# Kernel tuning notes

Hardware: AMD Instinct MI355X
Metric: run time of the kernel (lower is better)

The kernel has to match this reference:

```python
import jax, jax.numpy as jnp
import numpy as np

N = 200000      # nodes
E = 1600000     # edges
B = 1000        # graphs
SD = 64         # state_dim
AD = 32         # action_dim
H = 128         # HIDDEN_LAYER
EPS = 1e-5


def setup_inputs() -> dict:
    key = jax.random.key(0)
    ks = jax.random.split(key, 16)
    x = jax.random.normal(ks[0], (N, SD), dtype=jnp.float32)
    action = jax.random.normal(ks[1], (N, AD), dtype=jnp.float32)
    edge_index = jax.random.randint(ks[2], (2, E), 0, N, dtype=jnp.int64)
    batch_size = jnp.sort(jax.random.randint(ks[3], (N,), 0, B, dtype=jnp.int64))
    # parameters (Linear weights stored [in, out]; torch init std=0.1 for fc layers)
    W_gcn = jax.random.normal(ks[4], (SD, H), dtype=jnp.float32) / np.sqrt(SD)
    b_gcn = jnp.zeros((H,), jnp.float32)
    g0 = jnp.ones((H,), jnp.float32); be0 = jnp.zeros((H,), jnp.float32)
    W1 = jax.random.normal(ks[5], (H, H), dtype=jnp.float32) * 0.1
    b1 = jnp.zeros((H,), jnp.float32)
    g1 = jnp.ones((H,), jnp.float32); be1 = jnp.zeros((H,), jnp.float32)
    W2 = jax.random.normal(ks[6], (AD, H), dtype=jnp.float32) * 0.1
    b2 = jnp.zeros((H,), jnp.float32)
    g2 = jnp.ones((H,), jnp.float32); be2 = jnp.zeros((H,), jnp.float32)
    W3 = jax.random.normal(ks[7], (2 * H, 1), dtype=jnp.float32) * 0.1
    b3 = jnp.zeros((1,), jnp.float32)
    return dict(x=x, action=action, W_gcn=W_gcn, b_gcn=b_gcn, g0=g0, be0=be0,
                W1=W1, b1=b1, g1=g1, be1=be1, W2=W2, b2=b2, g2=g2, be2=be2,
                W3=W3, b3=b3, edge_index=edge_index, batch_size=batch_size)


def _bn(h, gamma, beta):
    # BatchNorm1d, training-mode batch statistics over the node axis
    mu = jnp.mean(h, axis=0)
    var = jnp.var(h, axis=0)
    return (h - mu) * jax.lax.rsqrt(var + EPS) * gamma + beta


def _gcn(x, edge_index, W, b):
    # GCN conv with self-loops and symmetric normalization:
    # out_i = sum_{j in N(i) u {i}} (d_i d_j)^{-1/2} (x_j W) + b
    loops = jnp.arange(N, dtype=edge_index.dtype)
    src = jnp.concatenate([edge_index[0], loops])
    dst = jnp.concatenate([edge_index[1], loops])
    deg = jax.ops.segment_sum(jnp.ones_like(dst, dtype=x.dtype), dst, num_segments=N)
    dinv = jax.lax.rsqrt(deg)                       # deg >= 1 due to self-loops
    norm = dinv[src] * dinv[dst]                    # [E+N]
    xw = x @ W                                      # [N, H]
    msg = xw[src] * norm[:, None]                   # [E+N, H]
    return jax.ops.segment_sum(msg, dst, num_segments=N) + b


def reference(x, action, W_gcn, b_gcn, g0, be0, W1, b1, g1, be1,
              W2, b2, g2, be2, W3, b3, edge_index, batch_size):
    h0 = jax.nn.relu(_gcn(x, edge_index, W_gcn, b_gcn))
    h0n = _bn(h0, g0, be0)
    h1 = jax.nn.relu(h0n @ W1 + b1)
    h1n = _bn(h1, g1, be1)
    h2 = jax.nn.relu(action @ W2 + b2)
    h2n = _bn(h2, g2, be2)
    feat = jnp.concatenate([h1n, h2n], axis=1)      # [N, 2H]
    sums = jax.ops.segment_sum(feat, batch_size, num_segments=B)
    cnts = jax.ops.segment_sum(jnp.ones((N,), feat.dtype), batch_size, num_segments=B)
    pooled = sums / jnp.maximum(cnts, 1.0)[:, None]  # [B, 2H]
    return pooled @ W3 + b3                          # [B, 1]
```

## Files before the change

### kernel.cpp

```cpp
#include <hip/hip_runtime.h>

typedef unsigned short u16;
typedef unsigned int   u32;
typedef __bf16 bf16x8 __attribute__((ext_vector_type(8)));
typedef float  f32x4  __attribute__((ext_vector_type(4)));

#define EPS 1e-5f
#define BSHIFT 9

__device__ __forceinline__ float b2f(u16 u){ union{u32 i; float f;} v; v.i=((u32)u)<<16; return v.f; }
__device__ __forceinline__ u16 f2b(float f){
  u32 x = __float_as_uint(f);
  u32 r = x + 0x7fffu + ((x>>16)&1u);
  return (u16)(r>>16);
}

template<int K, bool RELU, bool HASBIAS, bool AF32, bool POOL>
__device__ __forceinline__ void gemm_body(const void* __restrict__ Av,
                                          const u16* __restrict__ BhiT,
                                          const u16* __restrict__ BloT,
                                          const float* __restrict__ bias,
                                          u16* __restrict__ C,
                                          float* __restrict__ stats,
                                          const int* __restrict__ batch,
                                          float* __restrict__ P, int M,
                                          int bid, int halfg)
{
  constexpr int KM = K / 8;
  constexpr int KR = K / 32;
  extern __shared__ char smem[];
  u16* lds    = (u16*)smem;
  float* sred = (float*)(smem + (size_t)2 * 64 * K * 2);
  float* qred = sred + 64;
  const int tid = threadIdx.x;
  const int ch = (bid >= halfg) ? 1 : 0;
  const int t0 = bid - ch * halfg;
  for (int i = tid; i < 64 * KM; i += 256) {
    const int n = i / KM, kb = i % KM;
    const int kb2 = kb ^ (n & (KM - 1));
    const int gsrc = ((ch * 64 + n) * KM + kb) * 8;
    *(uint4*)(&lds[(n * KM + kb2) * 8])          = *(const uint4*)(BhiT + gsrc);
    *(uint4*)(&lds[64 * K + (n * KM + kb2) * 8]) = *(const uint4*)(BloT + gsrc);
  }
  if (tid < 64) { sred[tid] = 0.f; qred[tid] = 0.f; }
  __syncthreads();
  const int wid = tid >> 6, lane = tid & 63, q = lane >> 4, r16 = lane & 15;
  const int nmt = (M + 127) >> 7;
  float ls[4], lq[4];
#pragma unroll
  for (int nb = 0; nb < 4; nb++) { ls[nb] = 0.f; lq[nb] = 0.f; }
  float bv[4];
#pragma unroll
  for (int nb = 0; nb < 4; nb++) bv[nb] = HASBIAS ? bias[ch * 64 + nb * 16 + r16] : 0.f;

  for (int mt = t0; mt < nmt; mt += halfg) {
    const int row0 = mt << 7;
    const bool ok1 = (row0 + 64) < M;

    bf16x8 av[2][KR];
    if (AF32) {
      const float* Af = (const float*)Av + (size_t)(row0 + (wid << 4) + r16) * K + q * 8;
#pragma unroll
      for (int kk = 0; kk < KR; kk++) {
        f32x4 x0 = *(const f32x4*)(Af + kk * 32);
        f32x4 x1 = *(const f32x4*)(Af + kk * 32 + 4);
#pragma unroll
        for (int j = 0; j < 4; j++) { av[0][kk][j] = (__bf16)x0[j]; av[0][kk][4 + j] = (__bf16)x1[j]; }
      }
      if (ok1) {
        const float* Ag = Af + (size_t)64 * K;
#pragma unroll
        for (int kk = 0; kk < KR; kk++) {
          f32x4 x0 = *(const f32x4*)(Ag + kk * 32);
          f32x4 x1 = *(const f32x4*)(Ag + kk * 32 + 4);
#pragma unroll
          for (int j = 0; j < 4; j++) { av[1][kk][j] = (__bf16)x0[j]; av[1][kk][4 + j] = (__bf16)x1[j]; }
        }
      }
    } else {
      const u16* Ab = (const u16*)Av + (size_t)(row0 + (wid << 4) + r16) * K + q * 8;
#pragma unroll
      for (int kk = 0; kk < KR; kk++) av[0][kk] = *(const bf16x8*)(Ab + kk * 32);
      if (ok1) {
#pragma unroll
        for (int kk = 0; kk < KR; kk++) av[1][kk] = *(const bf16x8*)(Ab + (size_t)64 * K + kk * 32);
      }
    }

    f32x4 acc[2][4];
#pragma unroll
    for (int rt = 0; rt < 2; rt++)
#pragma unroll
      for (int nb = 0; nb < 4; nb++) acc[rt][nb] = (f32x4){0.f, 0.f, 0.f, 0.f};
#pragma unroll
    for (int kk = 0; kk < KR; kk++) {
#pragma unroll
      for (int nb = 0; nb < 4; nb++) {
        const int n = nb * 16 + r16;
        const int kb2 = (kk * 4 + q) ^ (n & (KM - 1));
        const bf16x8 bh = *(const bf16x8*)(&lds[(n * KM + kb2) * 8]);
        const bf16x8 bl = *(const bf16x8*)(&lds[64 * K + (n * KM + kb2) * 8]);
        acc[0][nb] = __builtin_amdgcn_mfma_f32_16x16x32_bf16(av[0][kk], bh, acc[0][nb], 0, 0, 0);
        acc[0][nb] = __builtin_amdgcn_mfma_f32_16x16x32_bf16(av[0][kk], bl, acc[0][nb], 0, 0, 0);
        if (ok1) {
          acc[1][nb] = __builtin_amdgcn_mfma_f32_16x16x32_bf16(av[1][kk], bh, acc[1][nb], 0, 0, 0);
          acc[1][nb] = __builtin_amdgcn_mfma_f32_16x16x32_bf16(av[1][kk], bl, acc[1][nb], 0, 0, 0);
        }
      }
    }

#pragma unroll
    for (int rt = 0; rt < 2; rt++) {
      if (rt && !ok1) continue;
      const int rbase = row0 + rt * 64 + (wid << 4) + (q << 2);
#pragma unroll
      for (int nb = 0; nb < 4; nb++) {
        const int col = ch * 64 + nb * 16 + r16;
#pragma unroll
        for (int r = 0; r < 4; r++) {
          float v = acc[rt][nb][r] + bv[nb];
          if (RELU) v = fmaxf(v, 0.f);
          ls[nb] += v; lq[nb] += v * v;
          if (!POOL) C[(size_t)(rbase + r) * 128 + col] = f2b(v);
          else acc[rt][nb][r] = v;
        }
      }
      if (POOL) {
        int bg[4];
#pragma unroll
        for (int r = 0; r < 4; r++) bg[r] = batch[rbase + r];
        const int g0 = __shfl(bg[0], 0, 64);
        const int g1 = __shfl(bg[3], 48, 64);
        for (int g = g0; g <= g1; ++g) {
#pragma unroll
          for (int nb = 0; nb < 4; nb++) {
            float sv = 0.f;
#pragma unroll
            for (int r = 0; r < 4; r++) sv += (bg[r] == g) ? acc[rt][nb][r] : 0.f;
            sv += __shfl_xor(sv, 16, 64);
            sv += __shfl_xor(sv, 32, 64);
            if (q == 0) atomicAdd(&P[g * 128 + ch * 64 + nb * 16 + r16], sv);
          }
        }
      }
    }
  }
#pragma unroll
  for (int nb = 0; nb < 4; nb++) {
    atomicAdd(&sred[nb * 16 + r16], ls[nb]);
    atomicAdd(&qred[nb * 16 + r16], lq[nb]);
  }
  __syncthreads();
  if (tid < 64) {
    atomicAdd(&stats[ch * 64 + tid], sred[tid]);
    atomicAdd(&stats[128 + ch * 64 + tid], qred[tid]);
  }
}

template<int K, bool RELU, bool HASBIAS, bool AF32, bool POOL>
__global__ __launch_bounds__(256) void k_gemm(const void* __restrict__ Av,
                                              const u16* __restrict__ BhiT,
                                              const u16* __restrict__ BloT,
                                              const float* __restrict__ bias,
                                              u16* __restrict__ C,
                                              float* __restrict__ stats,
                                              const int* __restrict__ batch,
                                              float* __restrict__ P, int M)
{
  gemm_body<K, RELU, HASBIAS, AF32, POOL>(Av, BhiT, BloT, bias, C, stats, batch, P, M,
                                          blockIdx.x, gridDim.x >> 1);
}

__global__ __launch_bounds__(256) void k_gemm2(const void* __restrict__ A1,
                                               const u16* __restrict__ B1hi,
                                               const u16* __restrict__ B1lo,
                                               const float* __restrict__ bias1,
                                               float* __restrict__ stats1,
                                               float* __restrict__ P1,
                                               const void* __restrict__ A2,
                                               const u16* __restrict__ B2hi,
                                               const u16* __restrict__ B2lo,
                                               const float* __restrict__ bias2,
                                               float* __restrict__ stats2,
                                               float* __restrict__ P2,
                                               const int* __restrict__ batch,
                                               int M, int g1blk, int g2blk)
{
  if ((int)blockIdx.x < g1blk)
    gemm_body<128, true, true, false, true>(A1, B1hi, B1lo, bias1, nullptr, stats1,
                                            batch, P1, M, blockIdx.x, g1blk >> 1);
  else
    gemm_body<32, true, true, true, true>(A2, B2hi, B2lo, bias2, nullptr, stats2,
                                          batch, P2, M, blockIdx.x - g1blk, g2blk >> 1);
}

__global__ void k_prep0(const float* __restrict__ Wg, const float* __restrict__ W2,
                        u16* __restrict__ WghiT, u16* __restrict__ WgloT,
                        u16* __restrict__ W2hiT, u16* __restrict__ W2loT,
                        const int* __restrict__ batch, int* __restrict__ gofs,
                        int* __restrict__ zbase, int zwords, int NZ, int N, int B)
{
  const int bid = blockIdx.x, t = threadIdx.x;
  if (bid < NZ) {
    const int i = bid * 2048 + t * 8;
    if (i < zwords) {
      *(int4*)(zbase + i)     = make_int4(0, 0, 0, 0);
      *(int4*)(zbase + i + 4) = make_int4(0, 0, 0, 0);
    }
  } else if (bid < NZ + 48) {
    const int i = (bid - NZ) * 256 + t;
    if (i < 64 * 128) {
      int k = i >> 7, n = i & 127;
      float w = Wg[i]; u16 h = f2b(w);
      WghiT[n * 64 + k] = h; WgloT[n * 64 + k] = f2b(w - b2f(h));
    } else if (i < 64 * 128 + 32 * 128) {
      int j = i - 64 * 128;
      int k = j >> 7, n = j & 127;
      float w = W2[j]; u16 h = f2b(w);
      W2hiT[n * 32 + k] = h; W2loT[n * 32 + k] = f2b(w - b2f(h));
    }
  } else {
    const int i = (bid - NZ - 48) * 256 + t;
    if (i == 0) { for (int g = 0; g <= batch[0]; g++) gofs[g] = 0; }
    if (i == N - 1) { for (int g = batch[N - 1] + 1; g <= B; g++) gofs[g] = N; }
    if (i < N - 1) {
      const int b0 = batch[i], b1 = batch[i + 1];
      for (int g = b0 + 1; g <= b1; g++) gofs[g] = i + 1;
    }
  }
}

__global__ __launch_bounds__(256) void k_bincnt(const int* __restrict__ dst, int* __restrict__ btot,
                                                int E, int NB)
{
  extern __shared__ int hist[];
  const int tid = threadIdx.x;
  for (int i = tid; i < NB; i += 256) hist[i] = 0;
  __syncthreads();
  const int chunk = (E + gridDim.x - 1) / gridDim.x;
  const int start = blockIdx.x * chunk;
  const int end = min(start + chunk, E);
  for (int e = start + tid; e < end; e += 256) atomicAdd(&hist[((u32)dst[e]) >> BSHIFT], 1);
  __syncthreads();
  for (int i = tid; i < NB; i += 256) if (hist[i]) atomicAdd(&btot[i], hist[i]);
}

__global__ void k_exscan(const int* __restrict__ in, int* __restrict__ out, int n)
{
  __shared__ int s[256];
  const int t = threadIdx.x;
  const int per = (n + 255) / 256;
  const int base = t * per;
  int loc[8]; int sum = 0;
  for (int j = 0; j < per; j++) { int v = (base + j < n) ? in[base + j] : 0; loc[j] = sum; sum += v; }
  s[t] = sum; __syncthreads();
  for (int o = 1; o < 256; o <<= 1) {
    int x = (t >= o) ? s[t - o] : 0;
    __syncthreads();
    s[t] += x;
    __syncthreads();
  }
  const int ex = s[t] - sum;
  for (int j = 0; j < per; j++) if (base + j < n) out[base + j] = ex + loc[j];
  if (t == 255) out[n] = s[255];
}

__global__ __launch_bounds__(256) void k_bin(const int* __restrict__ src, const int* __restrict__ dst,
                                             const int* __restrict__ bbase, int* __restrict__ bcur,
                                             uint2* __restrict__ pairs, int E, int NB)
{
  extern __shared__ int lds[];
  int* hist = lds; int* wbase = lds + NB;
  const int tid = threadIdx.x;
  for (int i = tid; i < NB; i += 256) hist[i] = 0;
  __syncthreads();
  const int chunk = (E + gridDim.x - 1) / gridDim.x;
  const int start = blockIdx.x * chunk;
  const int end = min(start + chunk, E);
  for (int e = start + tid; e < end; e += 256) atomicAdd(&hist[((u32)dst[e]) >> BSHIFT], 1);
  __syncthreads();
  for (int i = tid; i < NB; i += 256) {
    int c = hist[i];
    wbase[i] = c ? bbase[i] + atomicAdd(&bcur[i], c) : 0;
    hist[i] = 0;
  }
  __syncthreads();
  for (int e = start + tid; e < end; e += 256) {
    const int d = dst[e];
    const int b = ((u32)d) >> BSHIFT;
    const int o = atomicAdd(&hist[b], 1);
    pairs[wbase[b] + o] = make_uint2((u32)d, (u32)src[e]);
  }
}

__global__ __launch_bounds__(256) void k_bucket(const uint2* __restrict__ pairs,
                                                const int* __restrict__ bbase,
                                                const float* __restrict__ x,
                                                int* __restrict__ offsets, float* __restrict__ dinv,
                                                int* __restrict__ elist, u16* __restrict__ y,
                                                int N, int NB, int Etot)
{
  __shared__ int hist[512];
  __shared__ int scan[256];
  __shared__ int lcur[512];
  __shared__ float sdinv[512];
  const int b = blockIdx.x, t = threadIdx.x;
  const int nbase = b << BSHIFT;
  const int nn = min(1 << BSHIFT, N - nbase);
  hist[t] = 0; hist[256 + t] = 0;
  __syncthreads();
  const int p0 = bbase[b], p1 = bbase[b + 1];
  for (int p = p0 + t; p < p1; p += 256) atomicAdd(&hist[pairs[p].x - nbase], 1);
  __syncthreads();
  const int h0 = hist[2 * t], h1 = hist[2 * t + 1];
  const int psum = h0 + h1;
  scan[t] = psum; __syncthreads();
  for (int o = 1; o < 256; o <<= 1) {
    int xx = (t >= o) ? scan[t - o] : 0;
    __syncthreads();
    scan[t] += xx;
    __syncthreads();
  }
  const int ex = scan[t] - psum;
  const int li0 = 2 * t, li1 = 2 * t + 1;
  if (li0 < nn) {
    const int i = nbase + li0;
    const int off = p0 + ex + i;
    const float d = rsqrtf((float)(h0 + 1));
    offsets[i] = off; elist[off] = i; lcur[li0] = off + 1;
    dinv[i] = d; sdinv[li0] = d;
  }
  if (li1 < nn) {
    const int i = nbase + li1;
    const int off = p0 + ex + h0 + i;
    const float d = rsqrtf((float)(h1 + 1));
    offsets[i] = off; elist[off] = i; lcur[li1] = off + 1;
    dinv[i] = d; sdinv[li1] = d;
  }
  if (b == NB - 1 && t == 0) offsets[N] = Etot;
  __syncthreads();
  for (int p = p0 + t; p < p1; p += 256) {
    const uint2 pr = pairs[p];
    const int pos = atomicAdd(&lcur[pr.x - nbase], 1);
    elist[pos] = (int)pr.y;
  }
  const size_t ebase = (size_t)nbase * 64;
  const int total = nn * 64;
  for (int i = t * 8; i < total; i += 256 * 8) {
    const float d = sdinv[i >> 6];
    f32x4 a = *(const f32x4*)(x + ebase + i);
    f32x4 c = *(const f32x4*)(x + ebase + i + 4);
    u16 o[8];
#pragma unroll
    for (int j = 0; j < 4; j++) { o[j] = f2b(a[j] * d); o[4 + j] = f2b(c[j] * d); }
    *(uint4*)(y + ebase + i) = *(uint4*)o;
  }
}

__global__ __launch_bounds__(256) void k_agg(const u16* __restrict__ y, const int* __restrict__ offsets,
                                             const int* __restrict__ elist, const float* __restrict__ dinv,
                                             u16* __restrict__ aggx, int n)
{
  const int lane = threadIdx.x & 63;
  const int half = lane >> 5, l32 = lane & 31;
  const int g4 = l32 >> 3, sub = lane & 7;
  const int wid  = (blockIdx.x * 256 + threadIdx.x) >> 6;
  const int nw   = gridDim.x * 4;
  const int npair = (n + 1) >> 1;
  for (int pr = wid; pr < npair; pr += nw) {
    const int node = pr * 2 + half;
    const int s0 = offsets[node], s1 = offsets[node + 1];
    const int mydeg = s1 - s0;
    const int degA = __shfl(mydeg, 0, 64);
    const int degB = __shfl(mydeg, 32, 64);
    const int degmax = max(degA, degB);
    float a[8];
#pragma unroll
    for (int t = 0; t < 8; t++) a[t] = 0.f;
    for (int base = 0; base < degmax; base += 32) {
      const int m = mydeg - base;
      const int ev = (base + l32 < mydeg) ? elist[s0 + base + l32] : 0;
      const int iters = (min(32, degmax - base) + 3) >> 2;
      for (int it = 0; it < iters; it++) {
        const int j = it * 4 + g4;
        const int idx = __shfl(ev, half * 32 + j, 64);
        if (j < m) {
          const uint4 v = *(const uint4*)(y + (size_t)idx * 64 + sub * 8);
          const u32 w[4] = {v.x, v.y, v.z, v.w};
#pragma unroll
          for (int t = 0; t < 4; t++) {
            a[2 * t]     += b2f((u16)w[t]);
            a[2 * t + 1] += b2f((u16)(w[t] >> 16));
          }
        }
      }
    }
#pragma unroll
    for (int t = 0; t < 8; t++) {
      a[t] += __shfl_xor(a[t], 8, 64);
      a[t] += __shfl_xor(a[t], 16, 64);
    }
    if (g4 == 0) {
      const float di = dinv[node];
      u16 o[8];
#pragma unroll
      for (int t = 0; t < 8; t++) o[t] = f2b(a[t] * di);
      *(uint4*)(aggx + (size_t)node * 64 + sub * 8) = *(uint4*)o;
    }
  }
}

__global__ void k_prep1(const float* __restrict__ stats0, const float* __restrict__ W1,
                        const float* __restrict__ b1, const float* __restrict__ g0,
                        const float* __restrict__ be0, u16* __restrict__ W1hiT,
                        u16* __restrict__ W1loT, float* __restrict__ b1p, float n)
{
  __shared__ float A[8], Csh[8];
  const int t = threadIdx.x;
  if (t < 8) {
    const int k = blockIdx.x * 8 + t;
    const float mu = stats0[k] / n;
    const float var = fmaxf(stats0[128 + k] / n - mu * mu, 0.f);
    const float a = g0[k] * rsqrtf(var + EPS);
    A[t] = a; Csh[t] = be0[k] - mu * a;
  }
  __syncthreads();
  float acc = (blockIdx.x == 0) ? b1[t] : 0.f;
#pragma unroll
  for (int kk = 0; kk < 8; kk++) {
    const int k = blockIdx.x * 8 + kk;
    const float w0 = W1[k * 128 + t];
    acc += Csh[kk] * w0;
    const float w = A[kk] * w0;
    const u16 h = f2b(w);
    W1hiT[t * 128 + k] = h;
    W1loT[t * 128 + k] = f2b(w - b2f(h));
  }
  atomicAdd(&b1p[t], acc);
}

__global__ void k_out3(const float* __restrict__ P1, const float* __restrict__ P2,
                       const int* __restrict__ gofs,
                       const float* __restrict__ stats1, const float* __restrict__ stats2,
                       const float* __restrict__ g1, const float* __restrict__ be1,
                       const float* __restrict__ g2, const float* __restrict__ be2,
                       const float* __restrict__ W3, const float* __restrict__ b3,
                       float* __restrict__ out, int B, float n)
{
  __shared__ float w1s[128], w2s[128], red[256], cS[2];
  const int t = threadIdx.x;
  float c, wv;
  if (t < 128) {
    const float mu = stats1[t] / n;
    const float var = fmaxf(stats1[128 + t] / n - mu * mu, 0.f);
    const float a = g1[t] * rsqrtf(var + EPS);
    c = be1[t] - mu * a;
    wv = W3[t];
    w1s[t] = a * wv;
  } else {
    const int f = t - 128;
    const float mu = stats2[f] / n;
    const float var = fmaxf(stats2[128 + f] / n - mu * mu, 0.f);
    const float a = g2[f] * rsqrtf(var + EPS);
    c = be2[f] - mu * a;
    wv = W3[t];
    w2s[f] = a * wv;
  }
  red[t] = c * wv; __syncthreads();
  for (int o = 128; o; o >>= 1) { if (t < o) red[t] += red[t + o]; __syncthreads(); }
  if (t == 0) { cS[0] = red[0] + b3[0]; cS[1] = b3[0]; }
  __syncthreads();
  const int lane = t & 63;
  const int g = (blockIdx.x * 256 + t) >> 6;
  if (g >= B) return;
  const int cnt = gofs[g + 1] - gofs[g];
  const int k = 2 * lane;
  float d = P1[g * 128 + k] * w1s[k] + P1[g * 128 + k + 1] * w1s[k + 1]
          + P2[g * 128 + k] * w2s[k] + P2[g * 128 + k + 1] * w2s[k + 1];
#pragma unroll
  for (int o = 1; o < 64; o <<= 1) d += __shfl_xor(d, o, 64);
  if (lane == 0) out[g] = (cnt > 0) ? d / (float)cnt + cS[0] : cS[1];
}

extern "C" void kernel_launch(void* const* d_in, const int* in_sizes, int n_in,
                              void* d_out, int out_size, void* d_ws, size_t ws_size,
                              hipStream_t stream)
{
  const float* x    = (const float*)d_in[0];
  const float* act  = (const float*)d_in[1];
  const float* Wg   = (const float*)d_in[2];
  const float* bg   = (const float*)d_in[3];
  const float* g0   = (const float*)d_in[4];
  const float* be0  = (const float*)d_in[5];
  const float* W1   = (const float*)d_in[6];
  const float* b1   = (const float*)d_in[7];
  const float* g1   = (const float*)d_in[8];
  const float* be1  = (const float*)d_in[9];
  const float* W2   = (const float*)d_in[10];
  const float* b2   = (const float*)d_in[11];
  const float* g2   = (const float*)d_in[12];
  const float* be2  = (const float*)d_in[13];
  const float* W3   = (const float*)d_in[14];
  const float* b3   = (const float*)d_in[15];
  const int* eidx   = (const int*)d_in[16];
  const int* batch  = (const int*)d_in[17];

  const int N = in_sizes[17];
  const int E = in_sizes[16] / 2;
  const int B = out_size;
  const int* src = eidx;
  const int* dst = eidx + E;
  const int NB = (N + (1 << BSHIFT) - 1) >> BSHIFT;

  char* ws = (char*)d_ws;
  size_t off = 0;
  auto alloc = [&](size_t bytes) -> char* {
    off = (off + 255) & ~(size_t)255;
    char* p = ws + off; off += bytes; return p;
  };

  u16* bufA = (u16*)alloc((size_t)N * 128 * 2);
  u16* xb   = (u16*)alloc((size_t)N * 64 * 2);
  u16* aggx = (u16*)alloc((size_t)N * 64 * 2);

  int zwords = 768 + 128 + 2 * NB + 2 * 128 * B;
  zwords = (zwords + 7) & ~7;
  char* zbase   = alloc((size_t)zwords * 4);
  float* stats0 = (float*)zbase;
  float* stats1 = stats0 + 256;
  float* stats2 = stats1 + 256;
  float* b1p    = stats2 + 256;
  int*   btot   = (int*)(b1p + 128);
  int*   bcur   = btot + NB;
  float* P1     = (float*)(bcur + NB);
  float* P2     = P1 + 128 * B;

  int*   offsets = (int*)alloc((size_t)(N + 1) * 4);
  float* dinv    = (float*)alloc((size_t)N * 4);
  int*   elist   = (int*)alloc((size_t)(E + N) * 4);
  uint2* pairs   = (uint2*)alloc((size_t)E * 8);
  int*   bbase   = (int*)alloc((size_t)(NB + 1) * 4);
  int*   gofs    = (int*)alloc((size_t)(B + 1) * 4);
  u16*   WghiT   = (u16*)alloc(128 * 64 * 2);
  u16*   WgloT   = (u16*)alloc(128 * 64 * 2);
  u16*   W1hiT   = (u16*)alloc(128 * 128 * 2);
  u16*   W1loT   = (u16*)alloc(128 * 128 * 2);
  u16*   W2hiT   = (u16*)alloc(128 * 32 * 2);
  u16*   W2loT   = (u16*)alloc(128 * 32 * 2);

  u16* h0 = bufA;

  const int smem64  = 2 * 64 * 64 * 2 + 512;
  const int smem128 = 2 * 64 * 128 * 2 + 512;

  const int NZ = (zwords + 2047) / 2048;
  const int nbounds = (N + 255) / 256;
  k_prep0<<<NZ + 48 + nbounds, 256, 0, stream>>>(Wg, W2, WghiT, WgloT, W2hiT, W2loT,
                                                 batch, gofs, (int*)zbase, zwords, NZ, N, B);
  k_bincnt<<<256, 256, NB * 4, stream>>>(dst, btot, E, NB);
  k_exscan<<<1, 256, 0, stream>>>(btot, bbase, NB);
  k_bin<<<256, 256, 2 * NB * 4, stream>>>(src, dst, bbase, bcur, pairs, E, NB);
  k_bucket<<<NB, 256, 0, stream>>>(pairs, bbase, x, offsets, dinv, elist, xb, N, NB, E + N);
  k_agg<<<2048, 256, 0, stream>>>(xb, offsets, elist, dinv, aggx, N);
  k_gemm<64, true, true, false, false><<<768, 256, smem64, stream>>>(aggx, WghiT, WgloT, bg,
                                                                     h0, stats0, nullptr, nullptr, N);
  k_prep1<<<16, 128, 0, stream>>>(stats0, W1, b1, g0, be0, W1hiT, W1loT, b1p, (float)N);
  k_gemm2<<<768 + 512, 256, smem128, stream>>>(h0, W1hiT, W1loT, b1p, stats1, P1,
                                               act, W2hiT, W2loT, b2, stats2, P2,
                                               batch, N, 768, 512);
  k_out3<<<(B * 64 + 255) / 256, 256, 0, stream>>>(P1, P2, gofs, stats1, stats2,
                                                   g1, be1, g2, be2, W3, b3,
                                                   (float*)d_out, B, (float)N);
}
```

Measured before the change: 372.1 us.

## Accumulate graph pooling sums in LDS with contiguous tile ranges per block

In the pooled GEMM path, each block now processes a contiguous range of row tiles instead of a strided set. Before the main loop it stages that range's batch ids as u16 in shared memory. Per-graph partial sums for up to 8 graphs, starting at the block's first graph, are accumulated with shared-memory atomics and flushed to global memory once at the end. Graphs outside that window still fall back to global atomics. The aim is to cut global atomic traffic and contention on the pooled output and to avoid re-reading batch ids from global memory, at the cost of more shared memory and a possible change in load balance.

```diff
diff --git a/kernel.cpp b/kernel.cpp
--- a/kernel.cpp
+++ b/kernel.cpp
@@ -28,10 +28,13 @@
 {
   constexpr int KM = K / 8;
   constexpr int KR = K / 32;
+  constexpr int GCAP = 8;
   extern __shared__ char smem[];
   u16* lds    = (u16*)smem;
   float* sred = (float*)(smem + (size_t)2 * 64 * K * 2);
   float* qred = sred + 64;
+  u16*  sbatch = (u16*)(qred + 64);
+  float* Pacc  = (float*)(sbatch + 1024);
   const int tid = threadIdx.x;
   const int ch = (bid >= halfg) ? 1 : 0;
   const int t0 = bid - ch * halfg;
@@ -43,9 +46,23 @@
     *(uint4*)(&lds[64 * K + (n * KM + kb2) * 8]) = *(const uint4*)(BloT + gsrc);
   }
   if (tid < 64) { sred[tid] = 0.f; qred[tid] = 0.f; }
-  __syncthreads();
+  const int nmt = (M + 127) >> 7;
+  int mt_begin, mt_end, mt_step, rlo = 0;
+  if (POOL) {
+    const int qt = nmt / halfg, rm = nmt % halfg;
+    mt_begin = (t0 < rm) ? t0 * (qt + 1) : rm * (qt + 1) + (t0 - rm) * qt;
+    mt_end   = mt_begin + ((t0 < rm) ? qt + 1 : qt);
+    mt_step  = 1;
+    rlo = mt_begin << 7;
+    const int rcnt = min(mt_end << 7, M) - rlo;
+    for (int i = tid; i < rcnt; i += 256) sbatch[i] = (u16)batch[rlo + i];
+    for (int i = tid; i < GCAP * 64; i += 256) Pacc[i] = 0.f;
+  } else {
+    mt_begin = t0; mt_end = nmt; mt_step = halfg;
+  }
+  __syncthreads();
+  const int g_lo = POOL ? (int)sbatch[0] : 0;
   const int wid = tid >> 6, lane = tid & 63, q = lane >> 4, r16 = lane & 15;
-  const int nmt = (M + 127) >> 7;
   float ls[4], lq[4];
 #pragma unroll
   for (int nb = 0; nb < 4; nb++) { ls[nb] = 0.f; lq[nb] = 0.f; }
@@ -53,7 +70,7 @@
 #pragma unroll
   for (int nb = 0; nb < 4; nb++) bv[nb] = HASBIAS ? bias[ch * 64 + nb * 16 + r16] : 0.f;
 
-  for (int mt = t0; mt < nmt; mt += halfg) {
+  for (int mt = mt_begin; mt < mt_end; mt += mt_step) {
     const int row0 = mt << 7;
     const bool ok1 = (row0 + 64) < M;
 
@@ -128,7 +145,7 @@
       if (POOL) {
         int bg[4];
 #pragma unroll
-        for (int r = 0; r < 4; r++) bg[r] = batch[rbase + r];
+        for (int r = 0; r < 4; r++) bg[r] = (int)sbatch[rbase - rlo + r];
         const int g0 = __shfl(bg[0], 0, 64);
         const int g1 = __shfl(bg[3], 48, 64);
         for (int g = g0; g <= g1; ++g) {
@@ -139,7 +156,11 @@
             for (int r = 0; r < 4; r++) sv += (bg[r] == g) ? acc[rt][nb][r] : 0.f;
             sv += __shfl_xor(sv, 16, 64);
             sv += __shfl_xor(sv, 32, 64);
-            if (q == 0) atomicAdd(&P[g * 128 + ch * 64 + nb * 16 + r16], sv);
+            if (q == 0) {
+              const int gi = g - g_lo;
+              if ((unsigned)gi < GCAP) atomicAdd(&Pacc[gi * 64 + nb * 16 + r16], sv);
+              else atomicAdd(&P[g * 128 + ch * 64 + nb * 16 + r16], sv);
+            }
           }
         }
       }
@@ -154,6 +175,12 @@
   if (tid < 64) {
     atomicAdd(&stats[ch * 64 + tid], sred[tid]);
     atomicAdd(&stats[128 + ch * 64 + tid], qred[tid]);
+  }
+  if (POOL) {
+    for (int i = tid; i < GCAP * 64; i += 256) {
+      const float v = Pacc[i];
+      if (v != 0.f) atomicAdd(&P[(g_lo + (i >> 6)) * 128 + ch * 64 + (i & 63)], v);
+    }
   }
 }
 
@@ -551,7 +578,7 @@
   u16* h0 = bufA;
 
   const int smem64  = 2 * 64 * 64 * 2 + 512;
-  const int smem128 = 2 * 64 * 128 * 2 + 512;
+  const int smem128 = 2 * 64 * 128 * 2 + 512 + 2048 + 2048;
 
   const int NZ = (zwords + 2047) / 2048;
   const int nbounds = (N + 255) / 256;
```

Result: faster. 363.8 us, median of 2 (-2.2%).
